# Kernel tuning notes

Measured on AMD Instinct MI355X. Metric: run time of the kernel, lower is better.

## Reference

```python
import jax, jax.numpy as jnp
import numpy as np

THETA = 10000.0
EPS = 1e-6

def _rope_tables(n, d):
    # 2D image RoPE: square grid side x side, half of head-dim rotates with
    # row position, half with column position. rotate-half pairing (i, i+d/2).
    side = int(np.sqrt(n))
    dq = d // 4  # angle count per spatial axis
    inv_freq = 1.0 / (THETA ** (np.arange(dq, dtype=np.float32) / dq))
    ang = np.arange(side, dtype=np.float32)[:, None] * inv_freq[None, :]  # [side, dq]
    row = np.broadcast_to(ang[:, None, :], (side, side, dq)).reshape(n, dq)
    col = np.broadcast_to(ang[None, :, :], (side, side, dq)).reshape(n, dq)
    angles = np.concatenate([row, col], axis=-1)  # [n, d//2]
    return jnp.asarray(np.cos(angles)), jnp.asarray(np.sin(angles))

def _apply_rope(t, cos, sin):
    # t: [b, h, n, d]; cos/sin: [n, d//2]
    d2 = t.shape[-1] // 2
    t1, t2 = t[..., :d2], t[..., d2:]
    return jnp.concatenate([t1 * cos - t2 * sin, t1 * sin + t2 * cos], axis=-1)

def _rmsnorm(t, scale):
    var = jnp.mean(t * t, axis=-1, keepdims=True)
    return t * jax.lax.rsqrt(var + EPS) * scale

def setup_inputs() -> dict:
    key = jax.random.key(0)
    ks = jax.random.split(key, 3)
    B, N, D = 8, 1024, 1024
    x = jax.random.normal(ks[0], (B, N, D), dtype=jnp.float32)
    Wqkv = jax.random.normal(ks[1], (D, 3 * D), dtype=jnp.float32) * (D ** -0.5)
    bqkv = jnp.zeros((3 * D,), dtype=jnp.float32)
    Wout = jax.random.normal(ks[2], (D, D), dtype=jnp.float32) * (D ** -0.5)
    bout = jnp.zeros((D,), dtype=jnp.float32)
    hd = D // 16
    return {"x": x, "Wqkv": Wqkv, "bqkv": bqkv, "Wout": Wout, "bout": bout,
            "q_scale": jnp.ones((hd,), jnp.float32), "k_scale": jnp.ones((hd,), jnp.float32)}

def reference(x, Wqkv, bqkv, Wout, bout, q_scale, k_scale):
    B, N, D = x.shape
    H = 16
    hd = D // H
    qkv = x @ Wqkv + bqkv  # [B, N, 3D]
    qkv = qkv.reshape(B, N, 3, H, hd).transpose(2, 0, 3, 1, 4)  # [3, B, H, N, hd]
    q, k, v = qkv[0], qkv[1], qkv[2]
    q = _rmsnorm(q, q_scale)
    k = _rmsnorm(k, k_scale)
    cos, sin = _rope_tables(N, hd)
    q = _apply_rope(q, cos, sin)
    k = _apply_rope(k, cos, sin)
    scale = hd ** -0.5
    scores = jnp.einsum('bhqd,bhkd->bhqk', q, k) * scale
    attn = jax.nn.softmax(scores, axis=-1)
    o = jnp.einsum('bhqk,bhkd->bhqd', attn, v)  # [B, H, N, hd]
    o = o.transpose(0, 2, 1, 3).reshape(B, N, D)
    return o @ Wout + bout
```

## Files before the change

### kernel.cpp

```cpp
#include <hip/hip_runtime.h>
#include <hip/hip_bf16.h>
#include <hip/hip_fp16.h>
#include <math.h>

#define QSZ 8388608

typedef short bf16x8 __attribute__((ext_vector_type(8)));
typedef _Float16 f16x8 __attribute__((ext_vector_type(8)));
typedef float f32x4 __attribute__((ext_vector_type(4)));

__device__ __forceinline__ unsigned short f2bf(float f) {
  __hip_bfloat16 h = __float2bfloat16(f);
  return *reinterpret_cast<unsigned short*>(&h);
}

__device__ __forceinline__ void gload16(const void* g, void* l) {
  __builtin_amdgcn_global_load_lds(
      (const __attribute__((address_space(1))) void*)g,
      (__attribute__((address_space(3))) void*)l, 16, 0, 0);
}

__global__ __launch_bounds__(256)
void cvt_bf16(const float* __restrict__ src, unsigned short* __restrict__ dst) {
  const int i = (blockIdx.x * 256 + threadIdx.x) * 8;
  const float4 a = *(const float4*)&src[i];
  const float4 b = *(const float4*)&src[i + 4];
  ushort4 lo, hi;
  lo.x = f2bf(a.x); lo.y = f2bf(a.y); lo.z = f2bf(a.z); lo.w = f2bf(a.w);
  hi.x = f2bf(b.x); hi.y = f2bf(b.y); hi.z = f2bf(b.z); hi.w = f2bf(b.w);
  *(ushort4*)&dst[i] = lo;
  *(ushort4*)&dst[i + 4] = hi;
}

__global__ __launch_bounds__(256)
void cvt_t(const float* __restrict__ src, unsigned short* __restrict__ dst,
           const int N) {
  __shared__ unsigned short tile[32][33];
  const int k0 = blockIdx.y * 32, n0 = blockIdx.x * 32;
  const int t = threadIdx.x;
  const int r = t >> 3, c4 = (t & 7) * 4;
  const float4 v = *(const float4*)&src[(k0 + r) * N + n0 + c4];
  tile[r][c4 + 0] = f2bf(v.x);
  tile[r][c4 + 1] = f2bf(v.y);
  tile[r][c4 + 2] = f2bf(v.z);
  tile[r][c4 + 3] = f2bf(v.w);
  __syncthreads();
  ushort4 o;
  o.x = tile[c4 + 0][r];
  o.y = tile[c4 + 1][r];
  o.z = tile[c4 + 2][r];
  o.w = tile[c4 + 3][r];
  *(ushort4*)&dst[(long)(n0 + r) * 1024 + k0 + c4] = o;
}

template<int MODE, int GX>
__global__ __launch_bounds__(256)
void gemm_bf16(const unsigned short* __restrict__ A,
               const unsigned short* __restrict__ Bt,
               const float* __restrict__ bias, float* __restrict__ Cf,
               __half* __restrict__ Ch, const float* __restrict__ qsc,
               const float* __restrict__ ksc) {
  __shared__ __align__(16) unsigned short As[2][4096];
  __shared__ __align__(16) unsigned short Bs[2][4096];
  __shared__ float2 Tab[512];
  const int t = threadIdx.x;
  const int flat = blockIdx.x + blockIdx.y * GX;
  const int xcd = flat & 7, j = flat >> 3;
  const int bm = xcd * 8 + (j & 7), bn = j >> 3;
  const int w = t >> 6, lane = t & 63;
  const int wm = (w & 1) << 6, wn = (w >> 1) << 6;
  const int lm = lane & 15, lk = (lane >> 4) << 3;

  if (MODE == 0) {
    for (int e = t; e < 512; e += 256) {
      const int pos = e >> 4, idx = e & 15;
      const float invf = expf(-(float)idx * 0.57564627324851149f);
      const float ang = (float)pos * invf;
      Tab[e] = make_float2(cosf(ang), sinf(ang));
    }
  }

  const unsigned short* aptr =
      A + (long)(bm * 128 + (t >> 2)) * 1024 + ((t & 3) << 3);
  const unsigned short* bptr =
      Bt + (long)(bn * 128 + (t >> 2)) * 1024 + ((t & 3) << 3);

  f32x4 acc[4][4] = {};

  gload16(aptr, &As[0][t * 8]);
  gload16(aptr + 64 * 1024, &As[0][2048 + t * 8]);
  gload16(bptr, &Bs[0][t * 8]);
  gload16(bptr + 64 * 1024, &Bs[0][2048 + t * 8]);

  for (int it = 0; it < 32; ++it) {
    const int cur = it & 1;
    __syncthreads();
    if (it < 31) {
      const int nx = cur ^ 1;
      const int kk = (it + 1) * 32;
      gload16(aptr + kk, &As[nx][t * 8]);
      gload16(aptr + 64 * 1024 + kk, &As[nx][2048 + t * 8]);
      gload16(bptr + kk, &Bs[nx][t * 8]);
      gload16(bptr + 64 * 1024 + kk, &Bs[nx][2048 + t * 8]);
    }
    bf16x8 af[4], bfr[4];
#pragma unroll
    for (int mi = 0; mi < 4; ++mi)
      af[mi] = *(const bf16x8*)&As[cur][(wm + mi * 16 + lm) * 32 + lk];
#pragma unroll
    for (int ni = 0; ni < 4; ++ni)
      bfr[ni] = *(const bf16x8*)&Bs[cur][(wn + ni * 16 + lm) * 32 + lk];
#pragma unroll
    for (int mi = 0; mi < 4; ++mi)
#pragma unroll
      for (int ni = 0; ni < 4; ++ni)
        acc[mi][ni] = __builtin_amdgcn_mfma_f32_16x16x32_bf16(
            af[mi], bfr[ni], acc[mi][ni], 0, 0, 0);
  }

  const int r0 = (lane >> 4) << 2;
  const int nb = bn * 128 + wn;

  if (MODE == 1) {
#pragma unroll
    for (int mi = 0; mi < 4; ++mi)
#pragma unroll
      for (int ni = 0; ni < 4; ++ni) {
        const int n = nb + ni * 16 + lm;
        const float bv = bias[n];
#pragma unroll
        for (int r = 0; r < 4; ++r)
          Cf[(long)(bm * 128 + wm + mi * 16 + r0 + r) * 1024 + n] =
              acc[mi][ni][r] + bv;
      }
    return;
  }

  const int tq = nb >> 10, h = (nb >> 6) & 15;
  if (tq == 2) {
#pragma unroll
    for (int mi = 0; mi < 4; ++mi)
#pragma unroll
      for (int ni = 0; ni < 4; ++ni) {
        const int dd = ((nb + ni * 16 + lm) & 63);
        const float bv = bias[nb + ni * 16 + lm];
#pragma unroll
        for (int r = 0; r < 4; ++r) {
          const int m = bm * 128 + wm + mi * 16 + r0 + r;
          const int b = m >> 10, nn = m & 1023;
          Ch[2L * QSZ + ((long)((b * 16 + h) * 64 + dd)) * 1024 + nn] =
              __float2half(acc[mi][ni][r] + bv);
        }
      }
    return;
  }

  const float* scp = (tq == 0) ? qsc : ksc;
  const float qmul = (tq == 0) ? 0.125f : 1.0f;
  float scv[4], bv[4];
#pragma unroll
  for (int ni = 0; ni < 4; ++ni) {
    scv[ni] = scp[ni * 16 + lm];
    bv[ni] = bias[nb + ni * 16 + lm];
  }
  __half* base = Ch + (long)tq * QSZ;
#pragma unroll
  for (int mi = 0; mi < 4; ++mi) {
#pragma unroll
    for (int r = 0; r < 4; ++r) {
      const float v0 = acc[mi][0][r] + bv[0];
      const float v1 = acc[mi][1][r] + bv[1];
      const float v2 = acc[mi][2][r] + bv[2];
      const float v3 = acc[mi][3][r] + bv[3];
      float ss = v0 * v0 + v1 * v1 + v2 * v2 + v3 * v3;
      ss += __shfl_xor(ss, 1, 64);
      ss += __shfl_xor(ss, 2, 64);
      ss += __shfl_xor(ss, 4, 64);
      ss += __shfl_xor(ss, 8, 64);
      const float inv = rsqrtf(ss * (1.0f / 64.0f) + 1e-6f) * qmul;
      const float a0 = v0 * inv * scv[0];
      const float a1 = v1 * inv * scv[1];
      const float a2 = v2 * inv * scv[2];
      const float a3 = v3 * inv * scv[3];
      const int m = bm * 128 + wm + mi * 16 + r0 + r;
      const int b = m >> 10, nn = m & 1023;
      const float2 tr = Tab[(nn >> 5) * 16 + lm];
      const float2 tc = Tab[(nn & 31) * 16 + lm];
      __half* row = base + ((long)((b * 16 + h) * 1024 + nn)) * 64 + lm;
      row[0]  = __float2half(a0 * tr.x - a2 * tr.y);
      row[16] = __float2half(a1 * tc.x - a3 * tc.y);
      row[32] = __float2half(a0 * tr.y + a2 * tr.x);
      row[48] = __float2half(a1 * tc.y + a3 * tc.x);
    }
  }
}

__global__ __launch_bounds__(256)
void attn_mfma(const __half* __restrict__ qh, const __half* __restrict__ kh,
               const __half* __restrict__ vh, unsigned short* __restrict__ ob) {
  __shared__ __align__(16) __half Ks[2][4096];
  __shared__ __align__(16) __half Vs[2][4096];
  __shared__ __align__(16) __half Pl[4608];
  const int t = threadIdx.x;
  const int w = t >> 6, lane = t & 63;
  const int flat = blockIdx.x + blockIdx.y * 8;
  const int xcd = flat & 7, j = flat >> 3;
  const int bh = xcd * 16 + (j >> 3);
  const int qt = j & 7;
  const int lm = lane & 15, q4 = lane >> 4;

  f16x8 qf[2][2];
#pragma unroll
  for (int g = 0; g < 2; ++g) {
    const __half* qrow =
        qh + ((long)(bh * 1024 + qt * 128 + g * 64 + w * 16 + lm)) * 64 +
        q4 * 8;
    qf[g][0] = *(const f16x8*)qrow;
    qf[g][1] = *(const f16x8*)(qrow + 32);
  }

  f32x4 o[2][4] = {};
  float l_r[2][4] = {};

  const int prow = t >> 3, pc = t & 7;
  const int scz = pc ^ (prow & 7);
  const __half* ksrc0 = kh + (long)(bh * 1024 + prow) * 64 + scz * 8;
  const __half* vsrc0 = vh + (long)(bh * 64 + prow) * 1024 + scz * 8;
  __half* Pw = Pl + w * 1152;

  gload16(ksrc0, &Ks[0][t * 8]);
  gload16(ksrc0 + 32 * 64, &Ks[0][2048 + t * 8]);
  gload16(vsrc0, &Vs[0][t * 8]);
  gload16(vsrc0 + 32 * 1024, &Vs[0][2048 + t * 8]);

  for (int kc = 0; kc < 16; ++kc) {
    const int cur = kc & 1;
    __syncthreads();

    if (kc < 15) {
      const int nx = cur ^ 1;
      const __half* ksrc = ksrc0 + (kc + 1) * 4096;
      const __half* vsrc = vsrc0 + (kc + 1) * 64;
      gload16(ksrc, &Ks[nx][t * 8]);
      gload16(ksrc + 32 * 64, &Ks[nx][2048 + t * 8]);
      gload16(vsrc, &Vs[nx][t * 8]);
      gload16(vsrc + 32 * 1024, &Vs[nx][2048 + t * 8]);
    }

#pragma unroll
    for (int g = 0; g < 2; ++g) {
      f32x4 s[4];
#pragma unroll
      for (int nt = 0; nt < 4; ++nt) {
        s[nt] = (f32x4){0.f, 0.f, 0.f, 0.f};
        const int kr = nt * 16 + lm;
#pragma unroll
        for (int ks = 0; ks < 2; ++ks) {
          const f16x8 kf = *(const f16x8*)&Ks[cur][kr * 64 +
                                            (((ks << 2) + q4) ^ (kr & 7)) * 8];
          s[nt] = __builtin_amdgcn_mfma_f32_16x16x32_f16(qf[g][ks], kf, s[nt],
                                                         0, 0, 0);
        }
      }

#pragma unroll
      for (int nt = 0; nt < 4; ++nt) {
#pragma unroll
        for (int r = 0; r < 4; ++r) {
          const float p = __expf(s[nt][r] - 9.0f);
          l_r[g][r] += p;
          Pw[(q4 * 4 + r) * 72 + nt * 16 + lm] = (__half)p;
        }
      }

#pragma unroll
      for (int ks2 = 0; ks2 < 2; ++ks2) {
        const f16x8 pf = *(const f16x8*)&Pw[lm * 72 + ks2 * 32 + q4 * 8];
#pragma unroll
        for (int nt = 0; nt < 4; ++nt) {
          const int dr = nt * 16 + lm;
          const f16x8 vf = *(const f16x8*)&Vs[cur][dr * 64 +
                                           (((ks2 << 2) + q4) ^ (dr & 7)) * 8];
          o[g][nt] = __builtin_amdgcn_mfma_f32_16x16x32_f16(pf, vf, o[g][nt],
                                                            0, 0, 0);
        }
      }
    }
  }

  const int b = bh >> 4, h = bh & 15;
#pragma unroll
  for (int g = 0; g < 2; ++g) {
#pragma unroll
    for (int r = 0; r < 4; ++r) {
      float l = l_r[g][r];
      l += __shfl_xor(l, 1, 64);
      l += __shfl_xor(l, 2, 64);
      l += __shfl_xor(l, 4, 64);
      l += __shfl_xor(l, 8, 64);
      const float linv = 1.0f / l;
      const long rowg =
          (long)(b * 1024 + qt * 128 + g * 64 + w * 16 + q4 * 4 + r) * 1024 +
          h * 64;
#pragma unroll
      for (int nt = 0; nt < 4; ++nt)
        ob[rowg + nt * 16 + lm] = f2bf(o[g][nt][r] * linv);
    }
  }
}

extern "C" void kernel_launch(void* const* d_in, const int* in_sizes, int n_in,
                              void* d_out, int out_size, void* d_ws,
                              size_t ws_size, hipStream_t stream) {
  const float* x    = (const float*)d_in[0];
  const float* Wqkv = (const float*)d_in[1];
  const float* bqkv = (const float*)d_in[2];
  const float* Wout = (const float*)d_in[3];
  const float* bout = (const float*)d_in[4];
  const float* qs   = (const float*)d_in[5];
  const float* ks   = (const float*)d_in[6];
  float* out = (float*)d_out;
  float* W = (float*)d_ws;

  __half* qkvh = (__half*)W;
  __half* qpre = qkvh;
  __half* kpre = qkvh + QSZ;
  __half* vT   = qkvh + 2 * QSZ;
  unsigned short* xb  = (unsigned short*)(W + 12582912);
  unsigned short* ob  = xb;
  unsigned short* wqT = (unsigned short*)(W + 16777216);
  unsigned short* woT = wqT + 3 * 1024 * 1024;

  cvt_bf16<<<4096, 256, 0, stream>>>(x, xb);
  cvt_t<<<dim3(96, 32), 256, 0, stream>>>(Wqkv, wqT, 3072);
  cvt_t<<<dim3(32, 32), 256, 0, stream>>>(Wout, woT, 1024);
  gemm_bf16<0, 24><<<dim3(24, 64), 256, 0, stream>>>(xb, wqT, bqkv, nullptr,
                                                     qkvh, qs, ks);
  attn_mfma<<<dim3(8, 128), 256, 0, stream>>>(qpre, kpre, vT, ob);
  gemm_bf16<1, 8><<<dim3(8, 64), 256, 0, stream>>>(ob, woT, bout, out, nullptr,
                                                   nullptr, nullptr);
}
```

Measured before the change: 293.3 us.

## Split QKV projection into dedicated 256x256-tile GEMM with swizzled LDS

```diff
diff --git a/kernel.cpp b/kernel.cpp
--- a/kernel.cpp
+++ b/kernel.cpp
@@ -53,100 +53,112 @@
   *(ushort4*)&dst[(long)(n0 + r) * 1024 + k0 + c4] = o;
 }
 
-template<int MODE, int GX>
-__global__ __launch_bounds__(256)
-void gemm_bf16(const unsigned short* __restrict__ A,
-               const unsigned short* __restrict__ Bt,
-               const float* __restrict__ bias, float* __restrict__ Cf,
-               __half* __restrict__ Ch, const float* __restrict__ qsc,
-               const float* __restrict__ ksc) {
-  __shared__ __align__(16) unsigned short As[2][4096];
-  __shared__ __align__(16) unsigned short Bs[2][4096];
+__global__ __launch_bounds__(512, 2)
+void gemm_qkv(const unsigned short* __restrict__ A,
+              const unsigned short* __restrict__ Bt,
+              const float* __restrict__ bias,
+              __half* __restrict__ Ch,
+              const float* __restrict__ qsc,
+              const float* __restrict__ ksc) {
+  __shared__ __align__(16) unsigned short As[2][16384];
+  __shared__ __align__(16) unsigned short Bs[2][16384];
   __shared__ float2 Tab[512];
+
   const int t = threadIdx.x;
-  const int flat = blockIdx.x + blockIdx.y * GX;
-  const int xcd = flat & 7, j = flat >> 3;
-  const int bm = xcd * 8 + (j & 7), bn = j >> 3;
+  const int swz = (blockIdx.x & 7) * 48 + (blockIdx.x >> 3);
+  const int bm = swz / 12, bn = swz % 12;
   const int w = t >> 6, lane = t & 63;
-  const int wm = (w & 1) << 6, wn = (w >> 1) << 6;
-  const int lm = lane & 15, lk = (lane >> 4) << 3;
-
-  if (MODE == 0) {
-    for (int e = t; e < 512; e += 256) {
-      const int pos = e >> 4, idx = e & 15;
-      const float invf = expf(-(float)idx * 0.57564627324851149f);
-      const float ang = (float)pos * invf;
-      Tab[e] = make_float2(cosf(ang), sinf(ang));
-    }
-  }
-
-  const unsigned short* aptr =
-      A + (long)(bm * 128 + (t >> 2)) * 1024 + ((t & 3) << 3);
-  const unsigned short* bptr =
-      Bt + (long)(bn * 128 + (t >> 2)) * 1024 + ((t & 3) << 3);
-
-  f32x4 acc[4][4] = {};
-
-  gload16(aptr, &As[0][t * 8]);
-  gload16(aptr + 64 * 1024, &As[0][2048 + t * 8]);
-  gload16(bptr, &Bs[0][t * 8]);
-  gload16(bptr + 64 * 1024, &Bs[0][2048 + t * 8]);
-
-  for (int it = 0; it < 32; ++it) {
-    const int cur = it & 1;
-    __syncthreads();
-    if (it < 31) {
-      const int nx = cur ^ 1;
-      const int kk = (it + 1) * 32;
-      gload16(aptr + kk, &As[nx][t * 8]);
-      gload16(aptr + 64 * 1024 + kk, &As[nx][2048 + t * 8]);
-      gload16(bptr + kk, &Bs[nx][t * 8]);
-      gload16(bptr + 64 * 1024 + kk, &Bs[nx][2048 + t * 8]);
-    }
-    bf16x8 af[4], bfr[4];
-#pragma unroll
-    for (int mi = 0; mi < 4; ++mi)
-      af[mi] = *(const bf16x8*)&As[cur][(wm + mi * 16 + lm) * 32 + lk];
-#pragma unroll
-    for (int ni = 0; ni < 4; ++ni)
-      bfr[ni] = *(const bf16x8*)&Bs[cur][(wn + ni * 16 + lm) * 32 + lk];
-#pragma unroll
-    for (int mi = 0; mi < 4; ++mi)
-#pragma unroll
-      for (int ni = 0; ni < 4; ++ni)
-        acc[mi][ni] = __builtin_amdgcn_mfma_f32_16x16x32_bf16(
-            af[mi], bfr[ni], acc[mi][ni], 0, 0, 0);
-  }
-
-  const int r0 = (lane >> 4) << 2;
-  const int nb = bn * 128 + wn;
-
-  if (MODE == 1) {
-#pragma unroll
-    for (int mi = 0; mi < 4; ++mi)
+  const int M0 = (w >> 2) * 128, N0 = (w & 3) * 64;
+  const int lm = lane & 15, q4 = lane >> 4;
+
+  {
+    const int pos = t >> 4, idx = t & 15;
+    const float invf = expf(-(float)idx * 0.57564627324851149f);
+    const float ang = (float)pos * invf;
+    Tab[t] = make_float2(cosf(ang), sinf(ang));
+  }
+
+  const int c8 = ((t & 7) ^ ((t >> 3) & 7)) << 3;
+  const unsigned short* aSrc = A + (long)(bm * 256 + (t >> 3)) * 1024 + c8;
+  const unsigned short* bSrc = Bt + (long)(bn * 256 + (t >> 3)) * 1024 + c8;
+  unsigned short* lA[2] = {&As[0][t * 8], &As[1][t * 8]};
+  unsigned short* lB[2] = {&Bs[0][t * 8], &Bs[1][t * 8]};
+
+  f32x4 acc[8][4] = {};
+
+  auto stage = [&](int buf, int kt) {
+    const unsigned short* a = aSrc + kt * 64;
+    const unsigned short* b = bSrc + kt * 64;
+    unsigned short* la = lA[buf];
+    unsigned short* lb = lB[buf];
+#pragma unroll
+    for (int j = 0; j < 4; ++j) {
+      gload16(a + j * 65536, la + j * 4096);
+      gload16(b + j * 65536, lb + j * 4096);
+    }
+  };
+
+  auto compute = [&](const unsigned short* Ac, const unsigned short* Bc) {
+#pragma unroll
+    for (int kk = 0; kk < 2; ++kk) {
+      bf16x8 af[8], bg[4];
+#pragma unroll
+      for (int mi = 0; mi < 8; ++mi) {
+        const int row = M0 + mi * 16 + lm;
+        af[mi] = *(const bf16x8*)
+            &Ac[row * 64 + ((((kk << 2) + q4) ^ (row & 7)) << 3)];
+      }
 #pragma unroll
       for (int ni = 0; ni < 4; ++ni) {
-        const int n = nb + ni * 16 + lm;
-        const float bv = bias[n];
-#pragma unroll
-        for (int r = 0; r < 4; ++r)
-          Cf[(long)(bm * 128 + wm + mi * 16 + r0 + r) * 1024 + n] =
-              acc[mi][ni][r] + bv;
-      }
-    return;
-  }
-
+        const int row = N0 + ni * 16 + lm;
+        bg[ni] = *(const bf16x8*)
+            &Bc[row * 64 + ((((kk << 2) + q4) ^ (row & 7)) << 3)];
+      }
+#pragma unroll
+      for (int mi = 0; mi < 8; ++mi)
+#pragma unroll
+        for (int ni = 0; ni < 4; ++ni)
+          acc[mi][ni] = __builtin_amdgcn_mfma_f32_16x16x32_bf16(
+              af[mi], bg[ni], acc[mi][ni], 0, 0, 0);
+    }
+  };
+
+  stage(0, 0);
+  stage(1, 1);
+  asm volatile("s_waitcnt vmcnt(8)" ::: "memory");
+  __builtin_amdgcn_s_barrier();
+
+  for (int kt = 0; kt < 14; ++kt) {
+    const int s = kt & 1;
+    compute(s ? &As[1][0] : &As[0][0], s ? &Bs[1][0] : &Bs[0][0]);
+    asm volatile("s_waitcnt lgkmcnt(0)" ::: "memory");
+    __builtin_amdgcn_s_barrier();
+    stage(s, kt + 2);
+    asm volatile("s_waitcnt vmcnt(8)" ::: "memory");
+    __builtin_amdgcn_s_barrier();
+  }
+  compute(&As[0][0], &Bs[0][0]);
+  asm volatile("s_waitcnt lgkmcnt(0)" ::: "memory");
+  __builtin_amdgcn_s_barrier();
+  asm volatile("s_waitcnt vmcnt(0)" ::: "memory");
+  __builtin_amdgcn_s_barrier();
+  compute(&As[1][0], &Bs[1][0]);
+
+  const int r0 = q4 << 2;
+  const int nb = bn * 256 + N0;
   const int tq = nb >> 10, h = (nb >> 6) & 15;
+
   if (tq == 2) {
 #pragma unroll
-    for (int mi = 0; mi < 4; ++mi)
+    for (int mi = 0; mi < 8; ++mi)
 #pragma unroll
       for (int ni = 0; ni < 4; ++ni) {
-        const int dd = ((nb + ni * 16 + lm) & 63);
-        const float bv = bias[nb + ni * 16 + lm];
+        const int col = nb + ni * 16 + lm;
+        const int dd = col & 63;
+        const float bv = bias[col];
 #pragma unroll
         for (int r = 0; r < 4; ++r) {
-          const int m = bm * 128 + wm + mi * 16 + r0 + r;
+          const int m = bm * 256 + M0 + mi * 16 + r0 + r;
           const int b = m >> 10, nn = m & 1023;
           Ch[2L * QSZ + ((long)((b * 16 + h) * 64 + dd)) * 1024 + nn] =
               __float2half(acc[mi][ni][r] + bv);
@@ -165,7 +177,7 @@
   }
   __half* base = Ch + (long)tq * QSZ;
 #pragma unroll
-  for (int mi = 0; mi < 4; ++mi) {
+  for (int mi = 0; mi < 8; ++mi) {
 #pragma unroll
     for (int r = 0; r < 4; ++r) {
       const float v0 = acc[mi][0][r] + bv[0];
@@ -182,7 +194,7 @@
       const float a1 = v1 * inv * scv[1];
       const float a2 = v2 * inv * scv[2];
       const float a3 = v3 * inv * scv[3];
-      const int m = bm * 128 + wm + mi * 16 + r0 + r;
+      const int m = bm * 256 + M0 + mi * 16 + r0 + r;
       const int b = m >> 10, nn = m & 1023;
       const float2 tr = Tab[(nn >> 5) * 16 + lm];
       const float2 tc = Tab[(nn & 31) * 16 + lm];
@@ -193,6 +205,77 @@
       row[48] = __float2half(a1 * tc.y + a3 * tc.x);
     }
   }
+}
+
+template<int MODE, int GX>
+__global__ __launch_bounds__(256)
+void gemm_bf16(const unsigned short* __restrict__ A,
+               const unsigned short* __restrict__ Bt,
+               const float* __restrict__ bias, float* __restrict__ Cf,
+               __half* __restrict__ Ch, const float* __restrict__ qsc,
+               const float* __restrict__ ksc) {
+  __shared__ __align__(16) unsigned short As[2][4096];
+  __shared__ __align__(16) unsigned short Bs[2][4096];
+  const int t = threadIdx.x;
+  const int flat = blockIdx.x + blockIdx.y * GX;
+  const int xcd = flat & 7, j = flat >> 3;
+  const int bm = xcd * 8 + (j & 7), bn = j >> 3;
+  const int w = t >> 6, lane = t & 63;
+  const int wm = (w & 1) << 6, wn = (w >> 1) << 6;
+  const int lm = lane & 15, lk = (lane >> 4) << 3;
+
+  const unsigned short* aptr =
+      A + (long)(bm * 128 + (t >> 2)) * 1024 + ((t & 3) << 3);
+  const unsigned short* bptr =
+      Bt + (long)(bn * 128 + (t >> 2)) * 1024 + ((t & 3) << 3);
+
+  f32x4 acc[4][4] = {};
+
+  gload16(aptr, &As[0][t * 8]);
+  gload16(aptr + 64 * 1024, &As[0][2048 + t * 8]);
+  gload16(bptr, &Bs[0][t * 8]);
+  gload16(bptr + 64 * 1024, &Bs[0][2048 + t * 8]);
+
+  for (int it = 0; it < 32; ++it) {
+    const int cur = it & 1;
+    __syncthreads();
+    if (it < 31) {
+      const int nx = cur ^ 1;
+      const int kk = (it + 1) * 32;
+      gload16(aptr + kk, &As[nx][t * 8]);
+      gload16(aptr + 64 * 1024 + kk, &As[nx][2048 + t * 8]);
+      gload16(bptr + kk, &Bs[nx][t * 8]);
+      gload16(bptr + 64 * 1024 + kk, &Bs[nx][2048 + t * 8]);
+    }
+    bf16x8 af[4], bfr[4];
+#pragma unroll
+    for (int mi = 0; mi < 4; ++mi)
+      af[mi] = *(const bf16x8*)&As[cur][(wm + mi * 16 + lm) * 32 + lk];
+#pragma unroll
+    for (int ni = 0; ni < 4; ++ni)
+      bfr[ni] = *(const bf16x8*)&Bs[cur][(wn + ni * 16 + lm) * 32 + lk];
+#pragma unroll
+    for (int mi = 0; mi < 4; ++mi)
+#pragma unroll
+      for (int ni = 0; ni < 4; ++ni)
+        acc[mi][ni] = __builtin_amdgcn_mfma_f32_16x16x32_bf16(
+            af[mi], bfr[ni], acc[mi][ni], 0, 0, 0);
+  }
+
+  const int r0 = (lane >> 4) << 2;
+  const int nb = bn * 128 + wn;
+
+#pragma unroll
+  for (int mi = 0; mi < 4; ++mi)
+#pragma unroll
+    for (int ni = 0; ni < 4; ++ni) {
+      const int n = nb + ni * 16 + lm;
+      const float bvv = bias[n];
+#pragma unroll
+      for (int r = 0; r < 4; ++r)
+        Cf[(long)(bm * 128 + wm + mi * 16 + r0 + r) * 1024 + n] =
+            acc[mi][ni][r] + bvv;
+    }
 }
 
 __global__ __launch_bounds__(256)
@@ -334,8 +417,7 @@
   cvt_bf16<<<4096, 256, 0, stream>>>(x, xb);
   cvt_t<<<dim3(96, 32), 256, 0, stream>>>(Wqkv, wqT, 3072);
   cvt_t<<<dim3(32, 32), 256, 0, stream>>>(Wout, woT, 1024);
-  gemm_bf16<0, 24><<<dim3(24, 64), 256, 0, stream>>>(xb, wqT, bqkv, nullptr,
-                                                     qkvh, qs, ks);
+  gemm_qkv<<<384, 512, 0, stream>>>(xb, wqT, bqkv, qkvh, qs, ks);
   attn_mfma<<<dim3(8, 128), 256, 0, stream>>>(qpre, kpre, vT, ob);
   gemm_bf16<1, 8><<<dim3(8, 64), 256, 0, stream>>>(ob, woT, bout, out, nullptr,
                                                    nullptr, nullptr);
```

Result: faster. 275.1 us (-6.2%).
